# Kernel tuning notes

Hardware: AMD Instinct MI355X
Metric: run time of the kernel (lower is better)

Reference implementation:

```python
import jax, jax.numpy as jnp
import numpy as np

E, C, N, W_IN, W_OUT = 5, 2, 2048, 512, 256


def setup_inputs() -> dict:
    key = jax.random.key(0)
    ks = jax.random.split(key, 11)
    A = jax.random.uniform(ks[0], (E, N, N), dtype=jnp.float32)  # stacked edge-type adjacencies
    X = jax.random.normal(ks[1], (N, W_IN), dtype=jnp.float32)
    # GTConv weights (out_channels=C, in_channels=E), init std=0.01 as in torch
    gt_w0a = 0.01 * jax.random.normal(ks[2], (C, E), dtype=jnp.float32)
    gt_w0b = 0.01 * jax.random.normal(ks[3], (C, E), dtype=jnp.float32)
    gt_w1 = 0.01 * jax.random.normal(ks[4], (C, E), dtype=jnp.float32)
    gcn_w = jax.random.normal(ks[5], (W_IN, W_OUT), dtype=jnp.float32) / np.sqrt(W_IN)
    gcn_b = jnp.zeros((W_OUT,), dtype=jnp.float32)
    lin1_w = 0.02 * jax.random.normal(ks[6], (W_OUT, C * W_OUT), dtype=jnp.float32)
    lin1_b = jnp.zeros((W_OUT,), dtype=jnp.float32)
    lin2_w = 0.02 * jax.random.normal(ks[7], (W_OUT, W_OUT), dtype=jnp.float32)
    lin2_b = jnp.zeros((W_OUT,), dtype=jnp.float32)
    return {"A": A, "X": X, "gt_w0a": gt_w0a, "gt_w0b": gt_w0b, "gt_w1": gt_w1,
            "gcn_w": gcn_w, "gcn_b": gcn_b, "lin1_w": lin1_w, "lin1_b": lin1_b,
            "lin2_w": lin2_w, "lin2_b": lin2_b}


def _gtconv(w, A):
    # softmax over edge types, weighted sum of adjacencies == coalesce of scaled edge lists
    f = jax.nn.softmax(w, axis=1)  # (C, E)
    return jnp.einsum('ce,enm->cnm', f, A)  # (C, N, N)


def _normalize(H):
    # remove self loops, then divide each entry by its column (target) degree
    n = H.shape[-1]
    H = H * (1.0 - jnp.eye(n, dtype=H.dtype))
    deg = H.sum(axis=-2)                      # (C, N) column sums == scatter_add over col
    safe = jnp.where(deg != 0, deg, 1.0)
    dinv = jnp.where(deg != 0, 1.0 / safe, 0.0)
    return H * dinv[:, None, :]


def reference(A, X, gt_w0a, gt_w0b, gt_w1, gcn_w, gcn_b, lin1_w, lin1_b, lin2_w, lin2_b):
    # layer 0 (first=True): two GTConvs, per-channel spspmm == batched matmul
    Ha = _gtconv(gt_w0a, A)
    Hb = _gtconv(gt_w0b, A)
    H = _normalize(jnp.einsum('cij,cjk->cik', Ha, Hb))
    # layer 1 (first=False): H_ @ conv1(A)
    Hb2 = _gtconv(gt_w1, A)
    H = _normalize(jnp.einsum('cij,cjk->cik', H, Hb2))
    # GCNConv per channel: add self loops, symmetric deg^{-1/2} normalization, aggregate to col
    n = H.shape[-1]
    M = H + jnp.eye(n, dtype=H.dtype)         # (C, N, N)
    deg = M.sum(axis=-2)                      # (C, N)
    safe = jnp.where(deg > 0, deg, 1.0)
    dis = jnp.where(deg > 0, safe ** -0.5, 0.0)
    Ahat = dis[:, :, None] * M * dis[:, None, :]
    XW = X @ gcn_w                            # (N, W_OUT)
    out = jnp.einsum('crn,rf->cnf', Ahat, XW) + gcn_b  # out[c,n] = sum_r Ahat[c,r,n] XW[r]
    out = jax.nn.relu(out)                    # (C, N, W_OUT)
    Xcat = out.transpose(1, 0, 2).reshape(n, -1)       # concat channels along dim=1
    h = jax.nn.relu(Xcat @ lin1_w.T + lin1_b)
    return h @ lin2_w.T + lin2_b
```

## Files before the change

### kernel.cpp

```cpp
#include <hip/hip_runtime.h>
#include <cstdint>
#include <cstddef>

#define NN   2048
#define N2   (2048LL*2048LL)
#define CC   2
#define EE   5
#define WIN  512
#define WOUT 256

typedef __bf16 bf16_t;
typedef __attribute__((ext_vector_type(8))) __bf16 bf16x8;
typedef __attribute__((ext_vector_type(4))) __bf16 bf16x4;
typedef __attribute__((ext_vector_type(4))) float  f32x4;

__global__ void k_prep(const float* __restrict__ X, const float* __restrict__ l1w,
                       const float* __restrict__ l2w, const float* __restrict__ gcnw,
                       bf16_t* __restrict__ Xb, bf16_t* __restrict__ l1wb,
                       bf16_t* __restrict__ l2wb, bf16_t* __restrict__ gwT) {
  __shared__ bf16_t tile[64][65];
  int bid = blockIdx.x;
  if (bid < 608) {
    int i = bid * 256 + threadIdx.x;
    const float* src; bf16_t* dst; int off;
    if (i < 131072)      { src = X;   dst = Xb;   off = i; }
    else if (i < 147456) { src = l1w; dst = l1wb; off = i - 131072; }
    else if (i < 155648) { src = l2w; dst = l2wb; off = i - 147456; }
    else return;
    float4 a = ((const float4*)src)[off * 2];
    float4 b = ((const float4*)src)[off * 2 + 1];
    bf16x8 o;
    o[0] = (bf16_t)a.x; o[1] = (bf16_t)a.y; o[2] = (bf16_t)a.z; o[3] = (bf16_t)a.w;
    o[4] = (bf16_t)b.x; o[5] = (bf16_t)b.y; o[6] = (bf16_t)b.z; o[7] = (bf16_t)b.w;
    ((bf16x8*)dst)[off] = o;
  } else {
    int b2 = bid - 608;
    int m0 = (b2 & 7) * 64, n0 = (b2 >> 3) * 64;
    int t = threadIdx.x, tr = t >> 4, tc = (t & 15) << 2;
#pragma unroll
    for (int v = 0; v < 4; ++v) {
      int r = tr + v * 16;
      float4 d = *(const float4*)&gcnw[(long long)(m0 + r) * WOUT + n0 + tc];
      tile[r][tc + 0] = (bf16_t)d.x; tile[r][tc + 1] = (bf16_t)d.y;
      tile[r][tc + 2] = (bf16_t)d.z; tile[r][tc + 3] = (bf16_t)d.w;
    }
    __syncthreads();
#pragma unroll
    for (int v = 0; v < 4; ++v) {
      int r = tr + v * 16;
      bf16x4 o;
      o[0] = tile[tc + 0][r]; o[1] = tile[tc + 1][r];
      o[2] = tile[tc + 2][r]; o[3] = tile[tc + 3][r];
      *(bf16x4*)&gwT[(long long)(n0 + r) * WIN + m0 + tc] = o;
    }
  }
}


__global__ void k_combine(const float* __restrict__ A,
                          const float* __restrict__ w0a, const float* __restrict__ w0b,
                          const float* __restrict__ w1,
                          bf16_t* __restrict__ Ha, bf16_t* __restrict__ HbT,
                          bf16_t* __restrict__ Hb2T, float* __restrict__ part) {
  __shared__ bf16_t tl[2][64][65];
  __shared__ float cs[2][16][64];
  float f[3][2][5];
  {
    const float* wp[3] = {w0a, w0b, w1};
#pragma unroll
    for (int w = 0; w < 3; ++w)
#pragma unroll
      for (int c = 0; c < 2; ++c) {
        float x[5], m = -1e30f, s = 0.f;
#pragma unroll
        for (int e = 0; e < 5; ++e) { x[e] = wp[w][c * 5 + e]; m = fmaxf(m, x[e]); }
#pragma unroll
        for (int e = 0; e < 5; ++e) { x[e] = expf(x[e] - m); s += x[e]; }
#pragma unroll
        for (int e = 0; e < 5; ++e) f[w][c][e] = x[e] / s;
      }
  }
  int i0 = blockIdx.x * 64, j0 = blockIdx.y * 64;
  int t = threadIdx.x, tr = t >> 4, tc = (t & 15) << 2;
  float cs0[4] = {0, 0, 0, 0}, cs1[4] = {0, 0, 0, 0};
  bf16x4 hb2a[4], hb2b[4];

#pragma unroll
  for (int v = 0; v < 4; ++v) {
    int lr = tr + v * 16;
    long long gi = i0 + lr;
    const float* base = A + gi * (long long)NN + j0 + tc;
    float av[5][4];
#pragma unroll
    for (int e = 0; e < 5; ++e) {
      float4 q = *(const float4*)(base + (long long)e * N2);
      av[e][0] = q.x; av[e][1] = q.y; av[e][2] = q.z; av[e][3] = q.w;
    }
    bf16x4 ha0, ha1;
#pragma unroll
    for (int x = 0; x < 4; ++x) {
      float s0 = 0.f, s1 = 0.f, s2 = 0.f, s3 = 0.f, s4 = 0.f, s5 = 0.f;
#pragma unroll
      for (int e = 0; e < 5; ++e) {
        float u = av[e][x];
        s0 += f[0][0][e] * u; s1 += f[0][1][e] * u;
        s2 += f[1][0][e] * u; s3 += f[1][1][e] * u;
        s4 += f[2][0][e] * u; s5 += f[2][1][e] * u;
      }
      ha0[x] = (bf16_t)s0; cs0[x] += (float)ha0[x];
      ha1[x] = (bf16_t)s1; cs1[x] += (float)ha1[x];
      tl[0][lr][tc + x] = (bf16_t)s2; tl[1][lr][tc + x] = (bf16_t)s3;
      hb2a[v][x] = (bf16_t)s4; hb2b[v][x] = (bf16_t)s5;
    }
    *(bf16x4*)&Ha[0 * N2 + gi * NN + j0 + tc] = ha0;
    *(bf16x4*)&Ha[1 * N2 + gi * NN + j0 + tc] = ha1;
  }
#pragma unroll
  for (int x = 0; x < 4; ++x) { cs[0][tr][tc + x] = cs0[x]; cs[1][tr][tc + x] = cs1[x]; }
  __syncthreads();

#pragma unroll
  for (int v = 0; v < 4; ++v) {
    int lr = tr + v * 16;
#pragma unroll
    for (int ch = 0; ch < 2; ++ch) {
      bf16x4 o;
      o[0] = tl[ch][tc + 0][lr]; o[1] = tl[ch][tc + 1][lr];
      o[2] = tl[ch][tc + 2][lr]; o[3] = tl[ch][tc + 3][lr];
      *(bf16x4*)&HbT[(long long)ch * N2 + (long long)(j0 + lr) * NN + i0 + tc] = o;
    }
  }
  if (t < 128) {
    int ch = t >> 6, col = t & 63;
    float s = 0.f;
#pragma unroll
    for (int r = 0; r < 16; ++r) s += cs[ch][r][col];
    part[((long long)ch * 32 + blockIdx.x) * NN + j0 + col] = s;
  }
  __syncthreads();

#pragma unroll
  for (int v = 0; v < 4; ++v) {
    int lr = tr + v * 16;
#pragma unroll
    for (int x = 0; x < 4; ++x) {
      tl[0][lr][tc + x] = hb2a[v][x];
      tl[1][lr][tc + x] = hb2b[v][x];
    }
  }
  __syncthreads();

#pragma unroll
  for (int v = 0; v < 4; ++v) {
    int lr = tr + v * 16;
#pragma unroll
    for (int ch = 0; ch < 2; ++ch) {
      bf16x4 o;
      o[0] = tl[ch][tc + 0][lr]; o[1] = tl[ch][tc + 1][lr];
      o[2] = tl[ch][tc + 2][lr]; o[3] = tl[ch][tc + 3][lr];
      *(bf16x4*)&Hb2T[(long long)ch * N2 + (long long)(j0 + lr) * NN + i0 + tc] = o;
    }
  }
}

__global__ void k_s_finish(const float* __restrict__ part, float* __restrict__ s) {
  int idx = blockIdx.x * 256 + threadIdx.x;
  int c = idx >> 11, k = idx & 2047;
  float acc = 0.f;
#pragma unroll
  for (int ib = 0; ib < 32; ++ib) acc += part[((long long)c * 32 + ib) * NN + k];
  s[idx] = acc;
}

template<bool EMIT_DIS>
__global__ void k_deg(const float* __restrict__ svec, const bf16_t* __restrict__ Arows,
                      const bf16_t* __restrict__ BT,
                      float* __restrict__ out1, float* __restrict__ out2,
                      float* __restrict__ out3) {
  int c = blockIdx.y;
  int j = blockIdx.x * 4 + (threadIdx.x >> 6);
  int lane = threadIdx.x & 63;
  const bf16_t* a = Arows + (long long)c * N2 + (long long)j * NN;
  const bf16_t* b = BT + (long long)c * N2 + (long long)j * NN;
  const float* s = svec + c * NN;
  float acc_s = 0.f, acc_a = 0.f;
#pragma unroll
  for (int it = 0; it < 4; ++it) {
    int k0 = (lane + it * 64) * 8;
    bf16x8 av = *(const bf16x8*)(a + k0);
    bf16x8 bv = *(const bf16x8*)(b + k0);
    float4 s0 = *(const float4*)(s + k0);
    float4 s1 = *(const float4*)(s + k0 + 4);
    float sv[8] = {s0.x, s0.y, s0.z, s0.w, s1.x, s1.y, s1.z, s1.w};
#pragma unroll
    for (int x = 0; x < 8; ++x) {
      float bx = (float)bv[x];
      acc_s += sv[x] * bx;
      acc_a += (float)av[x] * bx;
    }
  }
#pragma unroll
  for (int o = 32; o > 0; o >>= 1) {
    acc_s += __shfl_xor(acc_s, o, 64);
    acc_a += __shfl_xor(acc_a, o, 64);
  }
  if (lane == 0) {
    float deg = acc_s - acc_a;
    bool nz = (deg != 0.f);
    if (!EMIT_DIS) {
      out1[c * NN + j] = nz ? 1.f / deg : 0.f;
      out2[c * NN + j] = nz ? 1.f : 0.f;
    } else {
      float dis = nz ? 0.70710678118654752f : 1.f;
      out1[c * NN + j] = nz ? dis / deg : 0.f;
      out2[c * NN + j] = dis;
      out3[c * NN + j] = acc_a;
    }
  }
}

__global__ void k_scale_xwd(const bf16_t* __restrict__ XWT, const float* __restrict__ disv,
                            bf16_t* __restrict__ XWdT) {
  int i = blockIdx.x * 256 + threadIdx.x;
  int c = i >> 16, rem = i & 65535;
  bf16x8 v = ((const bf16x8*)XWT)[rem];
  int col0 = (rem & 255) * 8;
  float4 d0 = *(const float4*)(disv + c * NN + col0);
  float4 d1 = *(const float4*)(disv + c * NN + col0 + 4);
  bf16x8 o;
  o[0] = (bf16_t)((float)v[0] * d0.x); o[1] = (bf16_t)((float)v[1] * d0.y);
  o[2] = (bf16_t)((float)v[2] * d0.z); o[3] = (bf16_t)((float)v[3] * d0.w);
  o[4] = (bf16_t)((float)v[4] * d1.x); o[5] = (bf16_t)((float)v[5] * d1.y);
  o[6] = (bf16_t)((float)v[6] * d1.z); o[7] = (bf16_t)((float)v[7] * d1.w);
  ((bf16x8*)XWdT)[i] = o;
}


enum { EP_F32 = 0, EP_NORM1T = 1, EP_BRELU = 3, EP_BF32 = 4, EP_XWT = 5, EP_BF16O = 7 };

template<int EP>
__global__ __launch_bounds__(256)
void k_gemm(const bf16_t* __restrict__ A, const bf16_t* __restrict__ B,
            void* __restrict__ Cv,
            const float* __restrict__ aux1, const float* __restrict__ aux2,
            bf16_t* __restrict__ aux3,
            int N, int K, int lda, int ldb,
            long long zA, long long zB, long long zC) {
  __shared__ __align__(16) char smem[36864];
  bf16_t* As = (bf16_t*)smem;
  bf16_t* Bs = (bf16_t*)(smem + 24576);
  bf16_t* tile = (bf16_t*)smem;

  int cz = blockIdx.z;
  const bf16_t* Ab = A + cz * zA + (long long)blockIdx.x * 128 * lda;
  const bf16_t* Bb = B + cz * zB + (long long)blockIdx.y * 64 * ldb;

  int t = threadIdx.x, wid = t >> 6, lane = t & 63;
  int wr = wid >> 1, wc = wid & 1;
  f32x4 acc[4][2] = {};
  int frow = lane & 15;
  int fk_sw = (((lane >> 4) ^ ((frow >> 1) & 3)) << 3);
  int srow = t >> 2;
  int scol_sw = (((t & 3) ^ ((t >> 3) & 3)) << 3);
  int nt = K >> 5;

  auto STAGE = [&](int TT, int BUF) {
    long long kko = (long long)TT * 32 + scol_sw;
    const bf16_t* ga0 = Ab + (long long)srow * lda + kko;
    const bf16_t* ga1 = Ab + (long long)(64 + srow) * lda + kko;
    const bf16_t* gb0 = Bb + (long long)srow * ldb + kko;
    char* la = smem + BUF * 8192 + wid * 1024;
    char* lb = smem + 24576 + BUF * 4096 + wid * 1024;
    __builtin_amdgcn_global_load_lds((__attribute__((address_space(1))) void*)ga0,
        (__attribute__((address_space(3))) void*)la, 16, 0, 0);
    __builtin_amdgcn_global_load_lds((__attribute__((address_space(1))) void*)ga1,
        (__attribute__((address_space(3))) void*)(la + 4096), 16, 0, 0);
    __builtin_amdgcn_global_load_lds((__attribute__((address_space(1))) void*)gb0,
        (__attribute__((address_space(3))) void*)lb, 16, 0, 0);
  };
  auto COMPUTE = [&](int BUF) {
    bf16x8 af[4], bfr[2];
#pragma unroll
    for (int m = 0; m < 4; ++m)
      af[m] = *(const bf16x8*)&As[BUF * 4096 + (wr * 64 + m * 16 + frow) * 32 + fk_sw];
#pragma unroll
    for (int n = 0; n < 2; ++n)
      bfr[n] = *(const bf16x8*)&Bs[BUF * 2048 + (wc * 32 + n * 16 + frow) * 32 + fk_sw];
#pragma unroll
    for (int m = 0; m < 4; ++m)
#pragma unroll
      for (int n = 0; n < 2; ++n)
        acc[m][n] = __builtin_amdgcn_mfma_f32_16x16x32_bf16(af[m], bfr[n], acc[m][n], 0, 0, 0);
  };

  STAGE(0, 0); STAGE(1, 1); STAGE(2, 2);
  int slot = 0;
  for (int tt = 0; tt < nt; ++tt) {
    int rem = nt - 1 - tt;
    if (rem >= 2)      asm volatile("s_waitcnt vmcnt(6)" ::: "memory");
    else if (rem == 1) asm volatile("s_waitcnt vmcnt(3)" ::: "memory");
    else               asm volatile("s_waitcnt vmcnt(0)" ::: "memory");
    __builtin_amdgcn_s_barrier();
    __builtin_amdgcn_sched_barrier(0);
    COMPUTE(slot);
    __builtin_amdgcn_s_barrier();
    if (tt + 3 < nt) STAGE(tt + 3, slot);
    slot = (slot == 2) ? 0 : slot + 1;
  }
  __builtin_amdgcn_sched_barrier(0);

  int rl0 = wr * 64 + ((lane >> 4) << 2);
  int cl0 = wc * 32 + (lane & 15);
  int r0 = blockIdx.x * 128 + rl0;
  int c0 = blockIdx.y * 64 + cl0;

  if constexpr (EP == EP_F32) {
    float* Cb = (float*)Cv + cz * zC;
#pragma unroll
    for (int m = 0; m < 4; ++m)
#pragma unroll
      for (int n = 0; n < 2; ++n)
#pragma unroll
        for (int j = 0; j < 4; ++j)
          Cb[(long long)(r0 + m * 16 + j) * N + c0 + n * 16] = acc[m][n][j];
  } else if constexpr (EP == EP_BF16O) {
    bf16_t* Cb = (bf16_t*)Cv + cz * zC;
#pragma unroll
    for (int m = 0; m < 4; ++m)
#pragma unroll
      for (int n = 0; n < 2; ++n)
#pragma unroll
        for (int j = 0; j < 4; ++j)
          Cb[(long long)(r0 + m * 16 + j) * N + c0 + n * 16] = (bf16_t)acc[m][n][j];
  } else if constexpr (EP == EP_NORM1T) {
    bf16_t* Cb = (bf16_t*)Cv + cz * zC;
    bf16_t* Ct = aux3 + cz * zC;
    float dj[2];
#pragma unroll
    for (int n = 0; n < 2; ++n) dj[n] = aux1[cz * NN + c0 + n * 16];
#pragma unroll
    for (int m = 0; m < 4; ++m)
#pragma unroll
      for (int n = 0; n < 2; ++n)
#pragma unroll
        for (int j = 0; j < 4; ++j) {
          int r = r0 + m * 16 + j, col = c0 + n * 16;
          float v = (r == col) ? 0.f : acc[m][n][j] * dj[n];
          Cb[(long long)r * NN + col] = (bf16_t)v;
          tile[(rl0 + m * 16 + j) * 65 + cl0 + n * 16] = (bf16_t)v;
        }
    __syncthreads();
    int nl = t >> 5, rl = (t & 31) * 4;
#pragma unroll
    for (int vv = 0; vv < 8; ++vv) {
      int n_l = nl + vv * 8;
      bf16x4 o;
      o[0] = tile[(rl + 0) * 65 + n_l]; o[1] = tile[(rl + 1) * 65 + n_l];
      o[2] = tile[(rl + 2) * 65 + n_l]; o[3] = tile[(rl + 3) * 65 + n_l];
      *(bf16x4*)&Ct[(long long)(blockIdx.y * 64 + n_l) * NN + blockIdx.x * 128 + rl] = o;
    }
  } else if constexpr (EP == EP_XWT) {
    float* Cb = (float*)Cv;
#pragma unroll
    for (int m = 0; m < 4; ++m)
#pragma unroll
      for (int n = 0; n < 2; ++n)
#pragma unroll
        for (int j = 0; j < 4; ++j) {
          float v = acc[m][n][j];
          Cb[(long long)(r0 + m * 16 + j) * N + c0 + n * 16] = v;
          tile[(rl0 + m * 16 + j) * 65 + cl0 + n * 16] = (bf16_t)v;
        }
    __syncthreads();
    int nl = t >> 5, rl = (t & 31) * 4;
#pragma unroll
    for (int vv = 0; vv < 8; ++vv) {
      int n_l = nl + vv * 8;
      bf16x4 o;
      o[0] = tile[(rl + 0) * 65 + n_l]; o[1] = tile[(rl + 1) * 65 + n_l];
      o[2] = tile[(rl + 2) * 65 + n_l]; o[3] = tile[(rl + 3) * 65 + n_l];
      *(bf16x4*)&aux3[(long long)(blockIdx.y * 64 + n_l) * NN + blockIdx.x * 128 + rl] = o;
    }
  } else if constexpr (EP == EP_BRELU) {
    bf16_t* Cb = (bf16_t*)Cv;
    float bj[2];
#pragma unroll
    for (int n = 0; n < 2; ++n) bj[n] = aux1[c0 + n * 16];
#pragma unroll
    for (int m = 0; m < 4; ++m)
#pragma unroll
      for (int n = 0; n < 2; ++n)
#pragma unroll
        for (int j = 0; j < 4; ++j)
          Cb[(long long)(r0 + m * 16 + j) * N + c0 + n * 16] =
              (bf16_t)fmaxf(acc[m][n][j] + bj[n], 0.f);
  } else {
    float* Cb = (float*)Cv;
    float bj[2];
#pragma unroll
    for (int n = 0; n < 2; ++n) bj[n] = aux1[c0 + n * 16];
#pragma unroll
    for (int m = 0; m < 4; ++m)
#pragma unroll
      for (int n = 0; n < 2; ++n)
#pragma unroll
        for (int j = 0; j < 4; ++j)
          Cb[(long long)(r0 + m * 16 + j) * N + c0 + n * 16] = acc[m][n][j] + bj[n];
  }
}


__global__ void k_gcn_epi2(const float* __restrict__ Z, const float* __restrict__ XW,
                           const float* __restrict__ gcn_b, const float* __restrict__ cscal,
                           const float* __restrict__ disv, const float* __restrict__ Mdiag,
                           bf16_t* __restrict__ Xcat) {
  long long idx4 = ((long long)blockIdx.x * 256 + threadIdx.x) * 4;
  int c = (int)(idx4 >> 19);
  int rem = (int)(idx4 & ((1 << 19) - 1));
  int n = rem >> 8, fcol = rem & 255;
  float4 z  = *(const float4*)(Z + (long long)c * NN * WOUT + rem);
  float4 xw = *(const float4*)(XW + rem);
  float4 b  = *(const float4*)(gcn_b + fcol);
  float cs = cscal[c * NN + n], dn = disv[c * NN + n], md = Mdiag[c * NN + n];
  float d2 = dn * dn, mdd = md * dn;
  bf16x4 o;
  o[0] = (bf16_t)fmaxf(cs * (z.x - mdd * xw.x) + d2 * xw.x + b.x, 0.f);
  o[1] = (bf16_t)fmaxf(cs * (z.y - mdd * xw.y) + d2 * xw.y + b.y, 0.f);
  o[2] = (bf16_t)fmaxf(cs * (z.z - mdd * xw.z) + d2 * xw.z + b.z, 0.f);
  o[3] = (bf16_t)fmaxf(cs * (z.w - mdd * xw.w) + d2 * xw.w + b.w, 0.f);
  *(bf16x4*)&Xcat[(long long)n * (CC * WOUT) + c * WOUT + fcol] = o;
}


extern "C" void kernel_launch(void* const* d_in, const int* in_sizes, int n_in,
                              void* d_out, int out_size, void* d_ws, size_t ws_size,
                              hipStream_t stream) {
  const float* A    = (const float*)d_in[0];
  const float* X    = (const float*)d_in[1];
  const float* w0a  = (const float*)d_in[2];
  const float* w0b  = (const float*)d_in[3];
  const float* w1   = (const float*)d_in[4];
  const float* gcnw = (const float*)d_in[5];
  const float* gcnb = (const float*)d_in[6];
  const float* l1w  = (const float*)d_in[7];
  const float* l1b  = (const float*)d_in[8];
  const float* l2w  = (const float*)d_in[9];
  const float* l2b  = (const float*)d_in[10];
  float* out = (float*)d_out;

  char* p = (char*)d_ws;
  auto carve = [&](size_t bytes) -> char* {
    char* r = p; p += (bytes + 255) & ~(size_t)255; return r;
  };
  float*  svec  = (float*)carve((size_t)CC * NN * 4);
  float*  dinv1 = (float*)carve((size_t)CC * NN * 4);
  float*  m1    = (float*)carve((size_t)CC * NN * 4);
  float*  cscal = (float*)carve((size_t)CC * NN * 4);
  float*  disv  = (float*)carve((size_t)CC * NN * 4);
  float*  Mdiag = (float*)carve((size_t)CC * NN * 4);
  float*  part  = (float*)carve((size_t)CC * 32 * NN * 4);
  bf16_t* S1    = (bf16_t*)carve((size_t)CC * N2 * 2);
  bf16_t* HbT   = (bf16_t*)carve((size_t)CC * N2 * 2);
  bf16_t* Hb2T  = (bf16_t*)carve((size_t)CC * N2 * 2);
  bf16_t* Hn    = (bf16_t*)carve((size_t)CC * N2 * 2);
  bf16_t* HnT   = (bf16_t*)carve((size_t)CC * N2 * 2);
  bf16_t* Xb    = (bf16_t*)carve((size_t)NN * WIN * 2);
  bf16_t* gwT   = (bf16_t*)carve((size_t)WOUT * WIN * 2);
  bf16_t* l1wb  = (bf16_t*)carve((size_t)WOUT * CC * WOUT * 2);
  bf16_t* l2wb  = (bf16_t*)carve((size_t)WOUT * WOUT * 2);
  float*  XW    = (float*)carve((size_t)NN * WOUT * 4);
  bf16_t* XWT   = (bf16_t*)carve((size_t)WOUT * NN * 2);
  bf16_t* Xcat  = (bf16_t*)carve((size_t)NN * CC * WOUT * 2);
  bf16_t* hb    = (bf16_t*)carve((size_t)NN * WOUT * 2);

  bf16_t* Ha = S1;
  bf16_t* XWdT = (bf16_t*)((char*)S1);
  bf16_t* Yt   = (bf16_t*)((char*)S1 + (2LL << 20));
  float*  Z    = (float*) ((char*)S1 + (6LL << 20));

  k_prep<<<640, 256, 0, stream>>>(X, l1w, l2w, gcnw, Xb, l1wb, l2wb, gwT);
  k_combine<<<dim3(32, 32), 256, 0, stream>>>(A, w0a, w0b, w1, Ha, HbT, Hb2T, part);
  k_s_finish<<<16, 256, 0, stream>>>(part, svec);

  k_deg<false><<<dim3(512, 2), 256, 0, stream>>>(svec, Ha, HbT, dinv1, m1, nullptr);
  k_gemm<EP_NORM1T><<<dim3(16, 32, 2), 256, 0, stream>>>(
      Ha, HbT, Hn, dinv1, nullptr, HnT, NN, NN, NN, NN, N2, N2, N2);

  k_deg<true><<<dim3(512, 2), 256, 0, stream>>>(m1, Hn, Hb2T, cscal, disv, Mdiag);

  k_gemm<EP_XWT><<<dim3(16, 4, 1), 256, 0, stream>>>(
      Xb, gwT, XW, nullptr, nullptr, XWT, WOUT, WIN, WIN, WIN, 0, 0, 0);
  k_scale_xwd<<<512, 256, 0, stream>>>(XWT, disv, XWdT);
  k_gemm<EP_BF16O><<<dim3(2, 32, 2), 256, 0, stream>>>(
      XWdT, HnT, Yt, nullptr, nullptr, nullptr, NN, NN, NN, NN,
      (long long)WOUT * NN, N2, (long long)WOUT * NN);
  k_gemm<EP_F32><<<dim3(16, 4, 2), 256, 0, stream>>>(
      Hb2T, Yt, Z, nullptr, nullptr, nullptr, WOUT, NN, NN, NN,
      N2, (long long)WOUT * NN, (long long)NN * WOUT);
  k_gcn_epi2<<<1024, 256, 0, stream>>>(Z, XW, gcnb, cscal, disv, Mdiag, Xcat);

  k_gemm<EP_BRELU><<<dim3(16, 4, 1), 256, 0, stream>>>(
      Xcat, l1wb, hb, l1b, nullptr, nullptr, WOUT, CC * WOUT, CC * WOUT, CC * WOUT, 0, 0, 0);
  k_gemm<EP_BF32><<<dim3(16, 4, 1), 256, 0, stream>>>(
      hb, l2wb, out, l2b, nullptr, nullptr, WOUT, WOUT, WOUT, WOUT, 0, 0, 0);
}
```

Baseline: 165.1 us.

## Use 128x128 tiled triple-buffered GEMM for first normalized adjacency product

Replaces the generic 128x64 GEMM with the NORM1T epilogue by a dedicated kernel that computes 128x128 output tiles per block, with a 4x4 MFMA accumulator per wave. Operands are staged through a three-slot LDS ring using direct global-to-LDS loads with explicit vmcnt waits. The larger tile halves the B re-reads and raises arithmetic intensity for the dominant 2048^3 batched matmul. In exchange the kernel uses more registers and 48KB of LDS, and launches half as many blocks (512), which may reduce occupancy.

```diff
diff --git a/kernel.cpp b/kernel.cpp
--- a/kernel.cpp
+++ b/kernel.cpp
@@ -236,7 +236,111 @@
 }
 
 
-enum { EP_F32 = 0, EP_NORM1T = 1, EP_BRELU = 3, EP_BF32 = 4, EP_XWT = 5, EP_BF16O = 7 };
+__global__ __launch_bounds__(256)
+void k_gemmL(const bf16_t* __restrict__ A, const bf16_t* __restrict__ B,
+             bf16_t* __restrict__ Hn, bf16_t* __restrict__ HnT,
+             const float* __restrict__ dinv) {
+  __shared__ __align__(16) char smem[49152];
+  bf16_t* As = (bf16_t*)smem;
+  bf16_t* Bs = (bf16_t*)(smem + 24576);
+  bf16_t* tile = (bf16_t*)smem;
+
+  int cz = blockIdx.z;
+  const bf16_t* Ab = A + cz * N2 + (long long)blockIdx.x * 128 * NN;
+  const bf16_t* Bb = B + cz * N2 + (long long)blockIdx.y * 128 * NN;
+
+  int t = threadIdx.x, wid = t >> 6, lane = t & 63;
+  int wr = wid >> 1, wc = wid & 1;
+  f32x4 acc[4][4] = {};
+  int frow = lane & 15;
+  int fk_sw = (((lane >> 4) ^ ((frow >> 1) & 3)) << 3);
+  int srow = t >> 2;
+  int scol_sw = (((t & 3) ^ ((t >> 3) & 3)) << 3);
+
+  auto STAGE = [&](int TT, int BUF) {
+    long long kko = (long long)TT * 32 + scol_sw;
+    const bf16_t* ga0 = Ab + (long long)srow * NN + kko;
+    const bf16_t* gb0 = Bb + (long long)srow * NN + kko;
+    char* la = smem + BUF * 8192 + wid * 1024;
+    char* lb = smem + 24576 + BUF * 8192 + wid * 1024;
+    __builtin_amdgcn_global_load_lds((__attribute__((address_space(1))) void*)ga0,
+        (__attribute__((address_space(3))) void*)la, 16, 0, 0);
+    __builtin_amdgcn_global_load_lds((__attribute__((address_space(1))) void*)(ga0 + 64LL * NN),
+        (__attribute__((address_space(3))) void*)(la + 4096), 16, 0, 0);
+    __builtin_amdgcn_global_load_lds((__attribute__((address_space(1))) void*)gb0,
+        (__attribute__((address_space(3))) void*)lb, 16, 0, 0);
+    __builtin_amdgcn_global_load_lds((__attribute__((address_space(1))) void*)(gb0 + 64LL * NN),
+        (__attribute__((address_space(3))) void*)(lb + 4096), 16, 0, 0);
+  };
+  auto COMPUTE = [&](int BUF) {
+    bf16x8 af[4], bfr[4];
+#pragma unroll
+    for (int m = 0; m < 4; ++m)
+      af[m] = *(const bf16x8*)&As[BUF * 4096 + (wr * 64 + m * 16 + frow) * 32 + fk_sw];
+#pragma unroll
+    for (int n = 0; n < 4; ++n)
+      bfr[n] = *(const bf16x8*)&Bs[BUF * 4096 + (wc * 64 + n * 16 + frow) * 32 + fk_sw];
+    __builtin_amdgcn_s_setprio(1);
+#pragma unroll
+    for (int m = 0; m < 4; ++m)
+#pragma unroll
+      for (int n = 0; n < 4; ++n)
+        acc[m][n] = __builtin_amdgcn_mfma_f32_16x16x32_bf16(af[m], bfr[n], acc[m][n], 0, 0, 0);
+    __builtin_amdgcn_s_setprio(0);
+  };
+
+  const int nt = 64;
+  STAGE(0, 0); STAGE(1, 1); STAGE(2, 2);
+  int slot = 0;
+  for (int tt = 0; tt < nt; ++tt) {
+    int rem = nt - 1 - tt;
+    if (rem >= 2)      asm volatile("s_waitcnt vmcnt(8)" ::: "memory");
+    else if (rem == 1) asm volatile("s_waitcnt vmcnt(4)" ::: "memory");
+    else               asm volatile("s_waitcnt vmcnt(0)" ::: "memory");
+    __builtin_amdgcn_s_barrier();
+    __builtin_amdgcn_sched_barrier(0);
+    COMPUTE(slot);
+    __builtin_amdgcn_s_barrier();
+    if (tt + 3 < nt) STAGE(tt + 3, slot);
+    slot = (slot == 2) ? 0 : slot + 1;
+  }
+  __builtin_amdgcn_sched_barrier(0);
+
+  int rl0 = wr * 64 + ((lane >> 4) << 2);
+  int cl0 = wc * 64 + (lane & 15);
+  int r0 = blockIdx.x * 128 + rl0;
+  int c0 = blockIdx.y * 128 + cl0;
+
+  bf16_t* Cb = Hn + cz * N2;
+  bf16_t* Ct = HnT + cz * N2;
+  float dj[4];
+#pragma unroll
+  for (int n = 0; n < 4; ++n) dj[n] = dinv[cz * NN + c0 + n * 16];
+#pragma unroll
+  for (int m = 0; m < 4; ++m)
+#pragma unroll
+    for (int n = 0; n < 4; ++n)
+#pragma unroll
+      for (int j = 0; j < 4; ++j) {
+        int r = r0 + m * 16 + j, col = c0 + n * 16;
+        float v = (r == col) ? 0.f : acc[m][n][j] * dj[n];
+        Cb[(long long)r * NN + col] = (bf16_t)v;
+        tile[(rl0 + m * 16 + j) * 130 + cl0 + n * 16] = (bf16_t)v;
+      }
+  __syncthreads();
+  int nl = t >> 5, rl = (t & 31) * 4;
+#pragma unroll
+  for (int vv = 0; vv < 16; ++vv) {
+    int n_l = nl + vv * 8;
+    bf16x4 o;
+    o[0] = tile[(rl + 0) * 130 + n_l]; o[1] = tile[(rl + 1) * 130 + n_l];
+    o[2] = tile[(rl + 2) * 130 + n_l]; o[3] = tile[(rl + 3) * 130 + n_l];
+    *(bf16x4*)&Ct[(long long)(blockIdx.y * 128 + n_l) * NN + blockIdx.x * 128 + rl] = o;
+  }
+}
+
+
+enum { EP_F32 = 0, EP_BRELU = 3, EP_BF32 = 4, EP_XWT = 5, EP_BF16O = 7 };
 
 template<int EP>
 __global__ __launch_bounds__(256)
@@ -332,33 +436,6 @@
 #pragma unroll
         for (int j = 0; j < 4; ++j)
           Cb[(long long)(r0 + m * 16 + j) * N + c0 + n * 16] = (bf16_t)acc[m][n][j];
-  } else if constexpr (EP == EP_NORM1T) {
-    bf16_t* Cb = (bf16_t*)Cv + cz * zC;
-    bf16_t* Ct = aux3 + cz * zC;
-    float dj[2];
-#pragma unroll
-    for (int n = 0; n < 2; ++n) dj[n] = aux1[cz * NN + c0 + n * 16];
-#pragma unroll
-    for (int m = 0; m < 4; ++m)
-#pragma unroll
-      for (int n = 0; n < 2; ++n)
-#pragma unroll
-        for (int j = 0; j < 4; ++j) {
-          int r = r0 + m * 16 + j, col = c0 + n * 16;
-          float v = (r == col) ? 0.f : acc[m][n][j] * dj[n];
-          Cb[(long long)r * NN + col] = (bf16_t)v;
-          tile[(rl0 + m * 16 + j) * 65 + cl0 + n * 16] = (bf16_t)v;
-        }
-    __syncthreads();
-    int nl = t >> 5, rl = (t & 31) * 4;
-#pragma unroll
-    for (int vv = 0; vv < 8; ++vv) {
-      int n_l = nl + vv * 8;
-      bf16x4 o;
-      o[0] = tile[(rl + 0) * 65 + n_l]; o[1] = tile[(rl + 1) * 65 + n_l];
-      o[2] = tile[(rl + 2) * 65 + n_l]; o[3] = tile[(rl + 3) * 65 + n_l];
-      *(bf16x4*)&Ct[(long long)(blockIdx.y * 64 + n_l) * NN + blockIdx.x * 128 + rl] = o;
-    }
   } else if constexpr (EP == EP_XWT) {
     float* Cb = (float*)Cv;
 #pragma unroll
@@ -483,8 +560,7 @@
   k_s_finish<<<16, 256, 0, stream>>>(part, svec);
 
   k_deg<false><<<dim3(512, 2), 256, 0, stream>>>(svec, Ha, HbT, dinv1, m1, nullptr);
-  k_gemm<EP_NORM1T><<<dim3(16, 32, 2), 256, 0, stream>>>(
-      Ha, HbT, Hn, dinv1, nullptr, HnT, NN, NN, NN, NN, N2, N2, N2);
+  k_gemmL<<<dim3(16, 16, 2), 256, 0, stream>>>(Ha, HbT, Hn, HnT, dinv1);
 
   k_deg<true><<<dim3(512, 2), 256, 0, stream>>>(m1, Hn, Hb2T, cscal, disv, Mdiag);
 
```

New measurement: 152.8 us. 1.08x faster.
